# Kernel optimization log

Measured on AMD Instinct MI355X. Metric: run time of the kernel, lower is better.

## Reference

```python
import jax, jax.numpy as jnp
import numpy as np

B, P, N, M = 8, 50, 128, 128          # batch, pomo, query nodes, route tokens
EMB, H, D = 128, 8, 16                # embedding_dim, head_num, qkv_dim
NE, K = 8, 2                          # num_experts, top-k
CLIP = 10.0                           # logit_clipping


def setup_inputs() -> dict:
    key = jax.random.key(0)
    ks = jax.random.split(key, 12)
    s = 0.02
    return {
        "encoded_nodes": jax.random.normal(ks[0], (B, P, N, EMB), jnp.float32),
        "encoded_routes": jax.random.normal(ks[1], (B, P, M, EMB + 1), jnp.float32),
        "ninf_mask": jnp.zeros((B, P, N), jnp.float32),
        "route_mask": jnp.zeros((B, P, N, M), jnp.float32),
        "Wq": s * jax.random.normal(ks[2], (EMB, H * D), jnp.float32),
        "Wk": s * jax.random.normal(ks[3], (EMB + 1, H * D), jnp.float32),
        "Wv": s * jax.random.normal(ks[4], (EMB + 1, H * D), jnp.float32),
        "Wg": s * jax.random.normal(ks[5], (H * D, NE), jnp.float32),
        "We": s * jax.random.normal(ks[6], (NE, H * D, EMB + 1), jnp.float32),
        "be": jnp.zeros((NE, EMB + 1), jnp.float32),
        "Wfinal": s * jax.random.normal(ks[7], (EMB + 1, 1), jnp.float32),
    }


def _heads(x, W):
    # x: [B,P,n,F] @ W[F,H*D] -> [B,P,H,n,D]
    y = x @ W
    b, p, n, _ = y.shape
    return jnp.swapaxes(y.reshape(b, p, n, H, D), 2, 3)


def reference(encoded_nodes, encoded_routes, ninf_mask, route_mask,
              Wq, Wk, Wv, Wg, We, be, Wfinal):
    # --- masked multi-head attention (multi_head_attention1) ---
    q = _heads(encoded_nodes, Wq)          # [B,P,H,N,D]
    k = _heads(encoded_routes, Wk)         # [B,P,H,M,D]
    v = _heads(encoded_routes, Wv)         # [B,P,H,M,D]
    score = jnp.einsum('bphnd,bphmd->bphnm', q, k) / jnp.sqrt(jnp.float32(D))
    score = score + route_mask[:, :, None, :, :]          # rank3 ninf mask
    w = jax.nn.softmax(score, axis=-1)
    # rank2 mask applied multiplicatively after softmax
    keep = jnp.where(ninf_mask == 0.0, 1.0, 0.0)[:, :, None, :, None]
    w = w * keep
    out = jnp.einsum('bphnm,bphmd->bphnd', w, v)
    out_concat = jnp.swapaxes(out, 2, 3).reshape(B, P, N, H * D)

    # --- top-k gated MoE combine (noisy gating, eval: no noise) ---
    x = out_concat.reshape(-1, H * D)                     # [T, H*D]
    T = x.shape[0]
    gate_logits = x @ Wg                                  # [T, NE]
    top_vals, top_idx = jax.lax.top_k(gate_logits, K)
    top_g = jax.nn.softmax(top_vals, axis=-1)
    gates = jnp.zeros((T, NE), x.dtype).at[jnp.arange(T)[:, None], top_idx].set(top_g)
    expert_out = jnp.einsum('ti,eio->teo', x, We) + be    # [T, NE, EMB+1]
    moe_out = jnp.einsum('te,teo->to', gates, expert_out)
    importance = gates.sum(0)
    moe_loss = importance.var() / (importance.mean() ** 2 + 1e-10)
    mh_atten_out = moe_out.reshape(B, P, N, EMB + 1)

    # --- final scoring ---
    score_scaled = (mh_atten_out @ Wfinal)[..., 0]        # [B,P,N]
    score_clipped = CLIP * jnp.tanh(score_scaled)
    score_masked = score_clipped + ninf_mask
    probs = jax.nn.softmax(score_masked, axis=2)
    return probs, moe_loss
```

## Files before the change

kernel.cpp:

```cpp
#include <hip/hip_runtime.h>

constexpr int B  = 8,  P = 50, N = 128, M = 128;
constexpr int EMB = 128, H = 8, D = 16;
constexpr int NE = 8;
constexpr int HD = H * D;
constexpr int E1 = EMB + 1;
constexpr int BP = B * P;
constexpr int T  = BP * N;

__global__ __launch_bounds__(256) void proj_kernel(
    const float* __restrict__ nodes,
    const float* __restrict__ routes,
    const float* __restrict__ Wq, const float* __restrict__ Wk,
    const float* __restrict__ Wv,
    float* __restrict__ qo, float* __restrict__ ko, float* __restrict__ vo,
    const float* __restrict__ We, const float* __restrict__ be,
    const float* __restrict__ Wf,
    float* __restrict__ Wep, float* __restrict__ bpv,
    float* __restrict__ importance, unsigned* __restrict__ ticket) {
    const int mat = blockIdx.y;

    if (mat == 3) {
        const int e = blockIdx.x;
        if (e >= NE) return;
        const int f = threadIdx.x;
        if (f < HD) {
            float a = 0.f;
            const long base = ((long)e * HD + f) * E1;
            for (int o = 0; o < E1; ++o) a += We[base + o] * Wf[o];
            Wep[e * HD + f] = a;
        } else if (f == HD) {
            float b = 0.f;
            for (int o = 0; o < E1; ++o) b += be[(long)e * E1 + o] * Wf[o];
            bpv[e] = b;
        }
        if (e == 0) {
            if (f >= 140 && f < 140 + NE) importance[f - 140] = 0.f;
            if (f == 150) *ticket = 0u;
        }
        return;
    }

    const float* __restrict__ X = (mat == 0) ? nodes : routes;
    const float* __restrict__ W = (mat == 0) ? Wq : (mat == 1 ? Wk : Wv);
    float* __restrict__ out     = (mat == 0) ? qo : (mat == 1 ? ko : vo);
    const int Kd = (mat == 0) ? EMB : E1;
    const int nit = (Kd + 7) >> 3;

    const int row0 = blockIdx.x * 128;
    const int tid  = threadIdx.x;
    const int tr   = tid >> 4;
    const int tc   = tid & 15;

    __shared__ float XT[2][8][132];
    __shared__ float WS[2][8][132];

    float acc[8][8];
    #pragma unroll
    for (int i = 0; i < 8; ++i)
        #pragma unroll
        for (int j = 0; j < 8; ++j) acc[i][j] = 0.f;

    float xr[4];
    float4 wr;
    const int xkx = tid & 7, xrr = tid >> 3;
    const int wkx = tid >> 5, wc4 = (tid & 31) * 4;

    {
        #pragma unroll
        for (int i = 0; i < 4; ++i) {
            int kg = xkx;
            xr[i] = (kg < Kd) ? X[(long)(row0 + xrr + i * 32) * Kd + kg] : 0.f;
        }
        wr = (wkx < Kd) ? *(const float4*)&W[(long)wkx * HD + wc4]
                        : make_float4(0.f, 0.f, 0.f, 0.f);
        #pragma unroll
        for (int i = 0; i < 4; ++i) XT[0][xkx][xrr + i * 32] = xr[i];
        *(float4*)&WS[0][wkx][wc4] = wr;
    }
    __syncthreads();

    for (int it = 0; it < nit; ++it) {
        const int buf = it & 1;
        if (it + 1 < nit) {
            const int kk = (it + 1) * 8;
            #pragma unroll
            for (int i = 0; i < 4; ++i) {
                int kg = kk + xkx;
                xr[i] = (kg < Kd) ? X[(long)(row0 + xrr + i * 32) * Kd + kg] : 0.f;
            }
            int kg = kk + wkx;
            wr = (kg < Kd) ? *(const float4*)&W[(long)kg * HD + wc4]
                           : make_float4(0.f, 0.f, 0.f, 0.f);
        }

        #pragma unroll
        for (int k = 0; k < 8; ++k) {
            float4 xa = *(const float4*)&XT[buf][k][tr * 4];
            float4 xb = *(const float4*)&XT[buf][k][64 + tr * 4];
            float4 wa = *(const float4*)&WS[buf][k][tc * 4];
            float4 wb = *(const float4*)&WS[buf][k][64 + tc * 4];
            float xv[8] = {xa.x, xa.y, xa.z, xa.w, xb.x, xb.y, xb.z, xb.w};
            float wvv[8] = {wa.x, wa.y, wa.z, wa.w, wb.x, wb.y, wb.z, wb.w};
            #pragma unroll
            for (int i = 0; i < 8; ++i)
                #pragma unroll
                for (int j = 0; j < 8; ++j) acc[i][j] += xv[i] * wvv[j];
        }

        if (it + 1 < nit) {
            const int nb = buf ^ 1;
            #pragma unroll
            for (int i = 0; i < 4; ++i) XT[nb][xkx][xrr + i * 32] = xr[i];
            *(float4*)&WS[nb][wkx][wc4] = wr;
        }
        __syncthreads();
    }

    #pragma unroll
    for (int i = 0; i < 8; ++i) {
        int r = row0 + (i < 4 ? 0 : 64) + tr * 4 + (i & 3);
        float4 o0 = make_float4(acc[i][0], acc[i][1], acc[i][2], acc[i][3]);
        float4 o1 = make_float4(acc[i][4], acc[i][5], acc[i][6], acc[i][7]);
        *(float4*)&out[(long)r * HD + tc * 4]      = o0;
        *(float4*)&out[(long)r * HD + 64 + tc * 4] = o1;
    }
}

__global__ __launch_bounds__(64) void attn_kernel(
    const float* __restrict__ qbuf,
    const float* __restrict__ kbuf,
    const float* __restrict__ vbuf,
    const float* __restrict__ rmask,
    const float* __restrict__ ninf,
    float* __restrict__ xcatT) {
    const int bp  = blockIdx.x;
    const int h   = blockIdx.y;
    const int tid = threadIdx.x;

    __shared__ float kh[M][D];

    #pragma unroll
    for (int i = 0; i < 8; ++i) {
        int e = tid + i * 64;
        int r = e >> 2, c4 = (e & 3) * 4;
        *(float4*)&kh[r][c4] = *(const float4*)&kbuf[((long)bp * M + r) * HD + h * D + c4];
    }
    __syncthreads();

    const long t0 = (long)bp * N + tid, t1 = t0 + 64;

    float qr0[16], qr1[16];
    {
        const float4* q0 = (const float4*)&qbuf[t0 * HD + h * D];
        const float4* q1 = (const float4*)&qbuf[t1 * HD + h * D];
        #pragma unroll
        for (int i = 0; i < 4; ++i) {
            float4 a = q0[i], b = q1[i];
            qr0[i*4+0] = a.x*0.25f; qr0[i*4+1] = a.y*0.25f;
            qr0[i*4+2] = a.z*0.25f; qr0[i*4+3] = a.w*0.25f;
            qr1[i*4+0] = b.x*0.25f; qr1[i*4+1] = b.y*0.25f;
            qr1[i*4+2] = b.z*0.25f; qr1[i*4+3] = b.w*0.25f;
        }
    }

    const float* __restrict__ vbase = vbuf + ((long)bp * M) * HD + h * D;
    const float4* rm0 = (const float4*)&rmask[t0 * M];
    const float4* rm1 = (const float4*)&rmask[t1 * M];

    float sum0 = 0.f, sum1 = 0.f;
    float o0[16], o1[16];
    #pragma unroll
    for (int d = 0; d < 16; ++d) { o0[d] = 0.f; o1[d] = 0.f; }

    for (int mb = 0; mb < 32; ++mb) {
        float4 r0 = rm0[mb], r1 = rm1[mb];
        float r0v[4] = {r0.x, r0.y, r0.z, r0.w};
        float r1v[4] = {r1.x, r1.y, r1.z, r1.w};
        #pragma unroll
        for (int j = 0; j < 4; ++j) {
            const int m = mb * 4 + j;
            const float4* k4 = (const float4*)&kh[m][0];
            const float4* v4 = (const float4*)&vbase[(long)m * HD];
            float s0 = 0.f, s1 = 0.f;
            #pragma unroll
            for (int q4 = 0; q4 < 4; ++q4) {
                float4 kq = k4[q4];
                s0 += qr0[q4*4+0]*kq.x + qr0[q4*4+1]*kq.y
                    + qr0[q4*4+2]*kq.z + qr0[q4*4+3]*kq.w;
                s1 += qr1[q4*4+0]*kq.x + qr1[q4*4+1]*kq.y
                    + qr1[q4*4+2]*kq.z + qr1[q4*4+3]*kq.w;
            }
            float e0 = __expf(s0 + r0v[j]);
            float e1 = __expf(s1 + r1v[j]);
            sum0 += e0; sum1 += e1;
            #pragma unroll
            for (int q4 = 0; q4 < 4; ++q4) {
                float4 vq = v4[q4];
                o0[q4*4+0] += e0*vq.x; o0[q4*4+1] += e0*vq.y;
                o0[q4*4+2] += e0*vq.z; o0[q4*4+3] += e0*vq.w;
                o1[q4*4+0] += e1*vq.x; o1[q4*4+1] += e1*vq.y;
                o1[q4*4+2] += e1*vq.z; o1[q4*4+3] += e1*vq.w;
            }
        }
    }

    const float inv0 = ((ninf[t0] == 0.f) ? 1.f : 0.f) / sum0;
    const float inv1 = ((ninf[t1] == 0.f) ? 1.f : 0.f) / sum1;
    float* __restrict__ xb = xcatT + (long)bp * HD * N + (long)h * D * N;
    #pragma unroll
    for (int d = 0; d < 16; ++d) {
        xb[d * N + tid]      = o0[d] * inv0;
        xb[d * N + tid + 64] = o1[d] * inv1;
    }
}

__global__ __launch_bounds__(128) void moe_final_kernel(
    const float* __restrict__ xcatT,
    const float* __restrict__ Wg,
    const float* __restrict__ ninf, const float* __restrict__ Wep,
    const float* __restrict__ bpv, float* __restrict__ importance,
    unsigned* __restrict__ ticket, float* __restrict__ out) {
    __shared__ float WgS[EMB][NE];
    __shared__ float WeS[NE][132];
    __shared__ float red[N];
    __shared__ float impS[NE];

    const int bp = blockIdx.x;
    const int n  = threadIdx.x;

    #pragma unroll
    for (int i = 0; i < 2; ++i) {
        int e = n + i * 128;
        int r = e >> 1, c4 = (e & 1) * 4;
        *(float4*)&WgS[r][c4] = *(const float4*)&Wg[(long)r * NE + c4];
    }
    #pragma unroll
    for (int i = 0; i < 2; ++i) {
        int idx = n + i * 128;
        int r = idx >> 5, c = (idx & 31) * 4;
        *(float4*)&WeS[r][c] = *(const float4*)&Wep[(long)r * HD + c];
    }
    if (n < NE) impS[n] = 0.f;
    __syncthreads();

    const long t = (long)bp * N + n;
    const float* __restrict__ xrow = xcatT + (long)bp * HD * N;

    float gl[NE];
    #pragma unroll
    for (int e = 0; e < NE; ++e) gl[e] = 0.f;
    for (int f = 0; f < HD; ++f) {
        float xv = xrow[f * N + n];
        #pragma unroll
        for (int e = 0; e < NE; ++e) gl[e] += xv * WgS[f][e];
    }

    int e0 = 0; float v0 = gl[0];
    #pragma unroll
    for (int e = 1; e < NE; ++e) if (gl[e] > v0) { v0 = gl[e]; e0 = e; }
    int e1 = -1; float v1 = -3.4e38f;
    #pragma unroll
    for (int e = 0; e < NE; ++e) if (e != e0 && gl[e] > v1) { v1 = gl[e]; e1 = e; }
    float ex = __expf(v1 - v0);
    float g0 = 1.f / (1.f + ex);
    float g1 = ex / (1.f + ex);

    atomicAdd(&impS[e0], g0);
    atomicAdd(&impS[e1], g1);

    float s = g0 * bpv[e0] + g1 * bpv[e1];
    for (int f = 0; f < HD; ++f) {
        float xv = xrow[f * N + n];
        s += xv * (g0 * WeS[e0][f] + g1 * WeS[e1][f]);
    }
    s = 10.f * tanhf(s) + ninf[t];

    red[n] = s;
    __syncthreads();
    for (int off = 64; off > 0; off >>= 1) {
        if (n < off) red[n] = fmaxf(red[n], red[n + off]);
        __syncthreads();
    }
    float mx = red[0];
    __syncthreads();
    float e = __expf(s - mx);
    red[n] = e;
    __syncthreads();
    for (int off = 64; off > 0; off >>= 1) {
        if (n < off) red[n] += red[n + off];
        __syncthreads();
    }
    float sum = red[0];

    out[t] = e / sum;

    if (n < NE) atomicAdd(&importance[n], impS[n]);

    __syncthreads();
    if (n == 0) {
        __threadfence();
        unsigned tk = atomicAdd(ticket, 1u);
        if (tk == BP - 1) {
            __threadfence();
            float imp[NE];
            #pragma unroll
            for (int ei = 0; ei < NE; ++ei)
                imp[ei] = atomicAdd(&importance[ei], 0.f);
            float mean = 0.f;
            #pragma unroll
            for (int ei = 0; ei < NE; ++ei) mean += imp[ei];
            mean *= (1.f / NE);
            float var = 0.f;
            #pragma unroll
            for (int ei = 0; ei < NE; ++ei) {
                float d = imp[ei] - mean;
                var += d * d;
            }
            var *= (1.f / NE);
            out[T] = var / (mean * mean + 1e-10f);
        }
    }
}

extern "C" void kernel_launch(void* const* d_in, const int* in_sizes, int n_in,
                              void* d_out, int out_size, void* d_ws, size_t ws_size,
                              hipStream_t stream) {
    const float* nodes  = (const float*)d_in[0];
    const float* routes = (const float*)d_in[1];
    const float* ninf   = (const float*)d_in[2];
    const float* rmask  = (const float*)d_in[3];
    const float* Wq     = (const float*)d_in[4];
    const float* Wk     = (const float*)d_in[5];
    const float* Wv     = (const float*)d_in[6];
    const float* Wg     = (const float*)d_in[7];
    const float* We     = (const float*)d_in[8];
    const float* be     = (const float*)d_in[9];
    const float* Wfin   = (const float*)d_in[10];

    float* ws = (float*)d_ws;
    float* Wep        = ws + 16;
    float* bpv        = ws + 1040;
    float* importance = ws + 1048;
    unsigned* ticket  = (unsigned*)(ws + 1056);
    float* qbuf       = ws + 4096;
    float* kbuf       = qbuf + (long)T * HD;
    float* vbuf       = kbuf + (long)T * HD;
    float* xcatT      = vbuf + (long)T * HD;

    float* out = (float*)d_out;

    proj_kernel<<<dim3(400, 4), 256, 0, stream>>>(nodes, routes, Wq, Wk, Wv,
                                                  qbuf, kbuf, vbuf,
                                                  We, be, Wfin, Wep, bpv,
                                                  importance, ticket);
    attn_kernel<<<dim3(BP, H), 64, 0, stream>>>(qbuf, kbuf, vbuf,
                                                rmask, ninf, xcatT);
    moe_final_kernel<<<BP, 128, 0, stream>>>(xcatT, Wg, ninf, Wep, bpv,
                                             importance, ticket, out);
}
```

Before: 286.1 us.

## Fuse MoE gating and final softmax into attention kernel via last-head ticket

```diff
diff --git a/kernel.cpp b/kernel.cpp
--- a/kernel.cpp
+++ b/kernel.cpp
@@ -17,7 +17,8 @@
     const float* __restrict__ We, const float* __restrict__ be,
     const float* __restrict__ Wf,
     float* __restrict__ Wep, float* __restrict__ bpv,
-    float* __restrict__ importance, unsigned* __restrict__ ticket) {
+    float* __restrict__ importance, unsigned* __restrict__ ticket,
+    unsigned* __restrict__ bpdone) {
     const int mat = blockIdx.y;
 
     if (mat == 3) {
@@ -38,6 +39,10 @@
             if (f >= 140 && f < 140 + NE) importance[f - 140] = 0.f;
             if (f == 150) *ticket = 0u;
         }
+        if (e == 1) {
+            bpdone[f] = 0u;
+            if (f < BP - 256) bpdone[f + 256] = 0u;
+        }
         return;
     }
 
@@ -127,24 +132,40 @@
     }
 }
 
-__global__ __launch_bounds__(64) void attn_kernel(
+__global__ __launch_bounds__(64) void attn_moe_kernel(
     const float* __restrict__ qbuf,
     const float* __restrict__ kbuf,
     const float* __restrict__ vbuf,
     const float* __restrict__ rmask,
     const float* __restrict__ ninf,
-    float* __restrict__ xcatT) {
+    const float* __restrict__ Wg,
+    const float* __restrict__ Wep,
+    const float* __restrict__ bpv,
+    float* __restrict__ importance,
+    unsigned* __restrict__ bpdone,
+    unsigned* __restrict__ ticket,
+    float* __restrict__ xcatT,
+    float* __restrict__ out) {
     const int bp  = blockIdx.x;
     const int h   = blockIdx.y;
     const int tid = threadIdx.x;
 
-    __shared__ float kh[M][D];
+    __shared__ union ShU {
+        float kh[M][D];
+        struct {
+            float Wg[EMB][NE];
+            float We[NE][132];
+            float red[64];
+            float imp[NE];
+        } moe;
+    } sh;
 
     #pragma unroll
     for (int i = 0; i < 8; ++i) {
         int e = tid + i * 64;
         int r = e >> 2, c4 = (e & 3) * 4;
-        *(float4*)&kh[r][c4] = *(const float4*)&kbuf[((long)bp * M + r) * HD + h * D + c4];
+        *(float4*)&sh.kh[r][c4] =
+            *(const float4*)&kbuf[((long)bp * M + r) * HD + h * D + c4];
     }
     __syncthreads();
 
@@ -180,7 +201,7 @@
         #pragma unroll
         for (int j = 0; j < 4; ++j) {
             const int m = mb * 4 + j;
-            const float4* k4 = (const float4*)&kh[m][0];
+            const float4* k4 = (const float4*)&sh.kh[m][0];
             const float4* v4 = (const float4*)&vbase[(long)m * HD];
             float s0 = 0.f, s1 = 0.f;
             #pragma unroll
@@ -213,92 +234,94 @@
         xb[d * N + tid]      = o0[d] * inv0;
         xb[d * N + tid + 64] = o1[d] * inv1;
     }
-}
-
-__global__ __launch_bounds__(128) void moe_final_kernel(
-    const float* __restrict__ xcatT,
-    const float* __restrict__ Wg,
-    const float* __restrict__ ninf, const float* __restrict__ Wep,
-    const float* __restrict__ bpv, float* __restrict__ importance,
-    unsigned* __restrict__ ticket, float* __restrict__ out) {
-    __shared__ float WgS[EMB][NE];
-    __shared__ float WeS[NE][132];
-    __shared__ float red[N];
-    __shared__ float impS[NE];
-
-    const int bp = blockIdx.x;
-    const int n  = threadIdx.x;
-
-    #pragma unroll
-    for (int i = 0; i < 2; ++i) {
-        int e = n + i * 128;
-        int r = e >> 1, c4 = (e & 1) * 4;
-        *(float4*)&WgS[r][c4] = *(const float4*)&Wg[(long)r * NE + c4];
-    }
-    #pragma unroll
-    for (int i = 0; i < 2; ++i) {
-        int idx = n + i * 128;
+
+    __syncthreads();
+    unsigned done = 0;
+    if (tid == 0) {
+        __threadfence();
+        done = atomicAdd(&bpdone[bp], 1u);
+    }
+    done = __shfl(done, 0);
+    if (done != H - 1) return;
+
+    __threadfence();
+    __syncthreads();
+
+    #pragma unroll
+    for (int i = 0; i < 4; ++i) {
+        int e4 = tid + i * 64;
+        int r = e4 >> 1, c4 = (e4 & 1) * 4;
+        *(float4*)&sh.moe.Wg[r][c4] = *(const float4*)&Wg[(long)r * NE + c4];
+    }
+    #pragma unroll
+    for (int i = 0; i < 4; ++i) {
+        int idx = tid + i * 64;
         int r = idx >> 5, c = (idx & 31) * 4;
-        *(float4*)&WeS[r][c] = *(const float4*)&Wep[(long)r * HD + c];
-    }
-    if (n < NE) impS[n] = 0.f;
-    __syncthreads();
-
-    const long t = (long)bp * N + n;
-    const float* __restrict__ xrow = xcatT + (long)bp * HD * N;
-
-    float gl[NE];
-    #pragma unroll
-    for (int e = 0; e < NE; ++e) gl[e] = 0.f;
-    for (int f = 0; f < HD; ++f) {
-        float xv = xrow[f * N + n];
-        #pragma unroll
-        for (int e = 0; e < NE; ++e) gl[e] += xv * WgS[f][e];
-    }
-
-    int e0 = 0; float v0 = gl[0];
-    #pragma unroll
-    for (int e = 1; e < NE; ++e) if (gl[e] > v0) { v0 = gl[e]; e0 = e; }
-    int e1 = -1; float v1 = -3.4e38f;
-    #pragma unroll
-    for (int e = 0; e < NE; ++e) if (e != e0 && gl[e] > v1) { v1 = gl[e]; e1 = e; }
-    float ex = __expf(v1 - v0);
-    float g0 = 1.f / (1.f + ex);
-    float g1 = ex / (1.f + ex);
-
-    atomicAdd(&impS[e0], g0);
-    atomicAdd(&impS[e1], g1);
-
-    float s = g0 * bpv[e0] + g1 * bpv[e1];
-    for (int f = 0; f < HD; ++f) {
-        float xv = xrow[f * N + n];
-        s += xv * (g0 * WeS[e0][f] + g1 * WeS[e1][f]);
-    }
-    s = 10.f * tanhf(s) + ninf[t];
-
-    red[n] = s;
-    __syncthreads();
-    for (int off = 64; off > 0; off >>= 1) {
-        if (n < off) red[n] = fmaxf(red[n], red[n + off]);
+        *(float4*)&sh.moe.We[r][c] = *(const float4*)&Wep[(long)r * HD + c];
+    }
+    if (tid < NE) sh.moe.imp[tid] = 0.f;
+    __syncthreads();
+
+    const float* __restrict__ xT = xcatT + (long)bp * HD * N;
+    float sv[2];
+    #pragma unroll
+    for (int half = 0; half < 2; ++half) {
+        const int tok = tid + half * 64;
+        float gl[NE];
+        #pragma unroll
+        for (int e = 0; e < NE; ++e) gl[e] = 0.f;
+        for (int f = 0; f < HD; ++f) {
+            float xv = xT[f * N + tok];
+            #pragma unroll
+            for (int e = 0; e < NE; ++e) gl[e] += xv * sh.moe.Wg[f][e];
+        }
+        int e0 = 0; float v0 = gl[0];
+        #pragma unroll
+        for (int e = 1; e < NE; ++e) if (gl[e] > v0) { v0 = gl[e]; e0 = e; }
+        int e1 = -1; float v1 = -3.4e38f;
+        #pragma unroll
+        for (int e = 0; e < NE; ++e) if (e != e0 && gl[e] > v1) { v1 = gl[e]; e1 = e; }
+        float ex = __expf(v1 - v0);
+        float g0 = 1.f / (1.f + ex);
+        float g1 = ex / (1.f + ex);
+
+        atomicAdd(&sh.moe.imp[e0], g0);
+        atomicAdd(&sh.moe.imp[e1], g1);
+
+        float s = g0 * bpv[e0] + g1 * bpv[e1];
+        for (int f = 0; f < HD; ++f) {
+            float xv = xT[f * N + tok];
+            s += xv * (g0 * sh.moe.We[e0][f] + g1 * sh.moe.We[e1][f]);
+        }
+        sv[half] = 10.f * tanhf(s) + ninf[(long)bp * N + tok];
+    }
+
+    sh.moe.red[tid] = fmaxf(sv[0], sv[1]);
+    __syncthreads();
+    for (int off = 32; off > 0; off >>= 1) {
+        if (tid < off) sh.moe.red[tid] = fmaxf(sh.moe.red[tid], sh.moe.red[tid + off]);
         __syncthreads();
     }
-    float mx = red[0];
-    __syncthreads();
-    float e = __expf(s - mx);
-    red[n] = e;
-    __syncthreads();
-    for (int off = 64; off > 0; off >>= 1) {
-        if (n < off) red[n] += red[n + off];
+    float mx = sh.moe.red[0];
+    __syncthreads();
+    float eA = __expf(sv[0] - mx);
+    float eB = __expf(sv[1] - mx);
+    sh.moe.red[tid] = eA + eB;
+    __syncthreads();
+    for (int off = 32; off > 0; off >>= 1) {
+        if (tid < off) sh.moe.red[tid] += sh.moe.red[tid + off];
         __syncthreads();
     }
-    float sum = red[0];
-
-    out[t] = e / sum;
-
-    if (n < NE) atomicAdd(&importance[n], impS[n]);
-
-    __syncthreads();
-    if (n == 0) {
+    float sum = sh.moe.red[0];
+
+    out[(long)bp * N + tid]      = eA / sum;
+    out[(long)bp * N + tid + 64] = eB / sum;
+
+    __syncthreads();
+    if (tid < NE) atomicAdd(&importance[tid], sh.moe.imp[tid]);
+
+    __syncthreads();
+    if (tid == 0) {
         __threadfence();
         unsigned tk = atomicAdd(ticket, 1u);
         if (tk == BP - 1) {
@@ -343,6 +366,7 @@
     float* bpv        = ws + 1040;
     float* importance = ws + 1048;
     unsigned* ticket  = (unsigned*)(ws + 1056);
+    unsigned* bpdone  = (unsigned*)(ws + 2048);
     float* qbuf       = ws + 4096;
     float* kbuf       = qbuf + (long)T * HD;
     float* vbuf       = kbuf + (long)T * HD;
@@ -353,9 +377,10 @@
     proj_kernel<<<dim3(400, 4), 256, 0, stream>>>(nodes, routes, Wq, Wk, Wv,
                                                   qbuf, kbuf, vbuf,
                                                   We, be, Wfin, Wep, bpv,
-                                                  importance, ticket);
-    attn_kernel<<<dim3(BP, H), 64, 0, stream>>>(qbuf, kbuf, vbuf,
-                                                rmask, ninf, xcatT);
-    moe_final_kernel<<<BP, 128, 0, stream>>>(xcatT, Wg, ninf, Wep, bpv,
-                                             importance, ticket, out);
+                                                  importance, ticket, bpdone);
+    attn_moe_kernel<<<dim3(BP, H), 64, 0, stream>>>(qbuf, kbuf, vbuf,
+                                                    rmask, ninf,
+                                                    Wg, Wep, bpv,
+                                                    importance, bpdone, ticket,
+                                                    xcatT, out);
 }
```

After: 391.1 us. +36.7%, slower.
